# Optimization experiments

Measured on AMD Instinct MI355X. Metric: run time of the kernel, lower is better.

## Reference

```python
import jax, jax.numpy as jnp
import numpy as np

B, N, M, NSAMPLE = 16, 16384, 1024, 32
RADIUS = 0.1


def setup_inputs() -> dict:
    key = jax.random.key(0)
    xyz = jax.random.uniform(key, (B, N, 3), dtype=jnp.float32)
    return {"xyz": xyz}


def _furthest_point_sample(xyz, m):
    # xyz: [B, N, 3] -> indices [B, m], sequential max-min-distance selection.
    b, n, _ = xyz.shape

    def step(carry, _):
        mindist, far = carry  # [B, N], [B]
        cent = jnp.take_along_axis(xyz, far[:, None, None], axis=1)  # [B,1,3]
        d = jnp.sum((xyz - cent) ** 2, axis=-1)  # [B, N]
        mindist = jnp.minimum(mindist, d)
        nxt = jnp.argmax(mindist, axis=-1).astype(jnp.int32)
        return (mindist, nxt), far

    init = (jnp.full((b, n), 1e10, dtype=xyz.dtype), jnp.zeros((b,), jnp.int32))
    _, idx = jax.lax.scan(step, init, None, length=m)  # [m, B]
    return idx.T  # [B, m]


def _ball_query(xyz, centroids, radius, nsample):
    # PointNet++ semantics: first `nsample` points (in index order) within
    # radius of each centroid; short lists padded with the first hit.
    n = xyz.shape[1]
    dist2 = jnp.sum((centroids[:, :, None, :] - xyz[:, None, :, :]) ** 2, axis=-1)  # [B,M,N]
    key = jnp.where(dist2 < radius * radius, jnp.arange(n, dtype=jnp.int32), n)
    # nsample smallest keys in ascending index order
    neg_top, _ = jax.lax.top_k(-key, nsample)
    idx = -neg_top  # [B, M, nsample], ascending
    valid = idx < n
    idx = jnp.where(valid, idx, idx[..., :1])  # pad with first hit
    return idx


def reference(xyz):
    fps_idx = _furthest_point_sample(xyz, M)  # [B, M]
    centroids = jnp.take_along_axis(xyz, fps_idx[..., None], axis=1)  # [B, M, 3]
    idx = _ball_query(xyz, centroids, RADIUS, NSAMPLE)  # [B, M, nsample]
    grouped = jax.vmap(lambda p, i: p[i])(xyz, idx)  # [B, M, nsample, 3]
    grouped = grouped - centroids[:, :, None, :]  # use_xyz=True relative coords
    return grouped, centroids
```

## Files before the change

kernel.cpp:

```cpp
#include <hip/hip_runtime.h>

#define BATCH 16
#define NPTS 16384
#define MCENT 1024
#define NSAMPLE 32

__global__ __launch_bounds__(1024) void fps_kernel(const float* __restrict__ xyz,
                                                   float* __restrict__ cent_out) {
#pragma clang fp contract(off)
    const int b = blockIdx.x;
    const int tid = threadIdx.x;
    const int lane = tid & 63;
    const int wid = tid >> 6;
    const float* xb = xyz + (size_t)b * NPTS * 3;
    float* cb = cent_out + (size_t)b * MCENT * 3;

    float px[16], py[16], pz[16], md[16];
#pragma unroll
    for (int j = 0; j < 16; ++j) {
        int p = j * 1024 + tid;
        px[j] = xb[p * 3 + 0];
        py[j] = xb[p * 3 + 1];
        pz[j] = xb[p * 3 + 2];
        md[j] = 1e10f;
    }

    __shared__ float redv[16];
    __shared__ int   redi[16];
    __shared__ int   cur_sh;

    int cur = 0;
    for (int m = 0; m < MCENT; ++m) {
        int c = __builtin_amdgcn_readfirstlane(cur);
        float cx = xb[c * 3 + 0];
        float cy = xb[c * 3 + 1];
        float cz = xb[c * 3 + 2];
        if (tid == 0) {
            cb[m * 3 + 0] = cx;
            cb[m * 3 + 1] = cy;
            cb[m * 3 + 2] = cz;
        }
        float bv = -1.0f;
        int bi = 0x7fffffff;
#pragma unroll
        for (int j = 0; j < 16; ++j) {
            float dx = px[j] - cx;
            float dy = py[j] - cy;
            float dz = pz[j] - cz;
            float d = dx * dx + dy * dy;
            d = d + dz * dz;
            float nm = fminf(md[j], d);
            md[j] = nm;
            if (nm > bv) { bv = nm; bi = j * 1024 + tid; }
        }
#pragma unroll
        for (int off = 32; off >= 1; off >>= 1) {
            float ov = __shfl_xor(bv, off);
            int   oi = __shfl_xor(bi, off);
            if (ov > bv || (ov == bv && oi < bi)) { bv = ov; bi = oi; }
        }
        if (lane == 0) { redv[wid] = bv; redi[wid] = bi; }
        __syncthreads();
        if (wid == 0) {
            float v = (lane < 16) ? redv[lane] : -1.0f;
            int   i = (lane < 16) ? redi[lane] : 0x7fffffff;
#pragma unroll
            for (int off = 8; off >= 1; off >>= 1) {
                float ov = __shfl_xor(v, off);
                int   oi = __shfl_xor(i, off);
                if (ov > v || (ov == v && oi < i)) { v = ov; i = oi; }
            }
            if (lane == 0) cur_sh = i;
        }
        __syncthreads();
        cur = cur_sh;
    }
}

__global__ __launch_bounds__(256) void ballq_kernel(const float* __restrict__ xyz,
                                                    const float* __restrict__ cent,
                                                    float* __restrict__ grouped) {
#pragma clang fp contract(off)
    const int lane = threadIdx.x & 63;
    const int wib = threadIdx.x >> 6;
    const int cid = blockIdx.x * 4 + wib;
    const int b = cid >> 10;
    const float* xb = xyz + (size_t)b * NPTS * 3;
    const float* c = cent + (size_t)cid * 3;
    float cx = c[0], cy = c[1], cz = c[2];
    float* g = grouped + (size_t)cid * NSAMPLE * 3;

    const float R2 = (float)(0.1 * 0.1);

    int total = 0;
    int first_p = -1;

    for (int p0 = 0; p0 < NPTS && total < NSAMPLE; p0 += 64) {
        int p = p0 + lane;
        float x = xb[p * 3 + 0];
        float y = xb[p * 3 + 1];
        float z = xb[p * 3 + 2];
        float dx = x - cx;
        float dy = y - cy;
        float dz = z - cz;
        float d = dx * dx + dy * dy;
        d = d + dz * dz;
        bool hit = d < R2;
        unsigned long long mask = __ballot(hit);
        if (hit) {
            unsigned int mb = __builtin_amdgcn_mbcnt_lo((unsigned int)mask, 0u);
            mb = __builtin_amdgcn_mbcnt_hi((unsigned int)(mask >> 32), mb);
            int pos = total + (int)mb;
            if (pos < NSAMPLE) {
                g[pos * 3 + 0] = dx;
                g[pos * 3 + 1] = dy;
                g[pos * 3 + 2] = dz;
            }
        }
        if (first_p < 0 && mask != 0ull) first_p = p0 + __builtin_ctzll(mask);
        total += __popcll(mask);
    }

    int sel = total < NSAMPLE ? total : NSAMPLE;
    if (sel < NSAMPLE) {
        float fx = xb[first_p * 3 + 0] - cx;
        float fy = xb[first_p * 3 + 1] - cy;
        float fz = xb[first_p * 3 + 2] - cz;
        int s = lane;
        if (s >= sel && s < NSAMPLE) {
            g[s * 3 + 0] = fx;
            g[s * 3 + 1] = fy;
            g[s * 3 + 2] = fz;
        }
    }
}

extern "C" void kernel_launch(void* const* d_in, const int* in_sizes, int n_in,
                              void* d_out, int out_size, void* d_ws, size_t ws_size,
                              hipStream_t stream) {
    const float* xyz = (const float*)d_in[0];
    float* out = (float*)d_out;
    float* grouped = out;
    float* cent = out + (size_t)BATCH * MCENT * NSAMPLE * 3;

    fps_kernel<<<BATCH, 1024, 0, stream>>>(xyz, cent);
    ballq_kernel<<<(BATCH * MCENT) / 4, 256, 0, stream>>>(xyz, cent, grouped);
}
```

Measured before the change: 2.626 ms.

## Morton-sort points and skip FPS updates for distant thread bounding boxes

Adds a per-batch Morton bucket sort that writes points (with original indices) into workspace so each thread owns a spatially compact group of 16 points. In FPS, each thread keeps a bounding box and skips the distance update when the box's lower-bound distance to the new centroid cannot lower its current max-min distance, and wavefronts with no active threads reuse their cached reduction result. The winning centroid's coordinates travel through the reduction, which drops a global load, and the reduction buffers are double-buffered so one barrier per iteration suffices. The cost is an extra kernel launch, extra shuffles per reduction step, and reliance on the 0.999 slack and index tie-breaks to keep selection identical to the reference.

```diff
diff --git a/kernel.cpp b/kernel.cpp
--- a/kernel.cpp
+++ b/kernel.cpp
@@ -4,76 +4,189 @@
 #define NPTS 16384
 #define MCENT 1024
 #define NSAMPLE 32
+#define PPT 16
+
+__device__ __forceinline__ unsigned morton10(float x, float y, float z) {
+    int qx = (int)(x * 16.0f); qx = qx < 0 ? 0 : (qx > 15 ? 15 : qx);
+    int qy = (int)(y * 8.0f);  qy = qy < 0 ? 0 : (qy > 7 ? 7 : qy);
+    int qz = (int)(z * 8.0f);  qz = qz < 0 ? 0 : (qz > 7 ? 7 : qz);
+    unsigned c = 0;
+    c |= (unsigned)(qx & 1) | ((unsigned)(qy & 1) << 1) | ((unsigned)(qz & 1) << 2);
+    c |= (((unsigned)(qx >> 1) & 1) << 3) | (((unsigned)(qy >> 1) & 1) << 4) | (((unsigned)(qz >> 1) & 1) << 5);
+    c |= (((unsigned)(qx >> 2) & 1) << 6) | (((unsigned)(qy >> 2) & 1) << 7) | (((unsigned)(qz >> 2) & 1) << 8);
+    c |= (((unsigned)(qx >> 3) & 1) << 9);
+    return c;
+}
+
+__global__ __launch_bounds__(1024) void sort_kernel(const float* __restrict__ xyz,
+                                                    float4* __restrict__ sorted) {
+    const int b = blockIdx.x;
+    const int tid = threadIdx.x;
+    const int lane = tid & 63;
+    const int wid = tid >> 6;
+    const float* xb = xyz + (size_t)b * NPTS * 3;
+    float4* sb = sorted + (size_t)b * NPTS;
+
+    __shared__ unsigned hist[1024];
+    __shared__ unsigned wsum[16];
+    hist[tid] = 0;
+    __syncthreads();
+
+    float mx[16], my[16], mz[16];
+    unsigned mc[16];
+#pragma unroll
+    for (int j = 0; j < 16; ++j) {
+        int p = j * 1024 + tid;
+        mx[j] = xb[p * 3 + 0];
+        my[j] = xb[p * 3 + 1];
+        mz[j] = xb[p * 3 + 2];
+        mc[j] = morton10(mx[j], my[j], mz[j]);
+        atomicAdd(&hist[mc[j]], 1u);
+    }
+    __syncthreads();
+
+    unsigned orig = hist[tid];
+    unsigned v = orig;
+#pragma unroll
+    for (int off = 1; off < 64; off <<= 1) {
+        unsigned n = __shfl_up(v, off);
+        if (lane >= off) v += n;
+    }
+    if (lane == 63) wsum[wid] = v;
+    __syncthreads();
+    if (wid == 0 && lane < 16) {
+        unsigned s = wsum[lane];
+#pragma unroll
+        for (int off = 1; off < 16; off <<= 1) {
+            unsigned n = __shfl_up(s, off);
+            if (lane >= off) s += n;
+        }
+        wsum[lane] = s;
+    }
+    __syncthreads();
+    unsigned base = v - orig + (wid > 0 ? wsum[wid - 1] : 0u);
+    __syncthreads();
+    hist[tid] = base;
+    __syncthreads();
+
+#pragma unroll
+    for (int j = 0; j < 16; ++j) {
+        int p = j * 1024 + tid;
+        unsigned pos = atomicAdd(&hist[mc[j]], 1u);
+        sb[pos] = make_float4(mx[j], my[j], mz[j], __int_as_float(p));
+    }
+}
 
 __global__ __launch_bounds__(1024) void fps_kernel(const float* __restrict__ xyz,
+                                                   const float4* __restrict__ sorted,
                                                    float* __restrict__ cent_out) {
 #pragma clang fp contract(off)
     const int b = blockIdx.x;
     const int tid = threadIdx.x;
     const int lane = tid & 63;
     const int wid = tid >> 6;
+    const float4* sb = sorted + (size_t)b * NPTS;
     const float* xb = xyz + (size_t)b * NPTS * 3;
     float* cb = cent_out + (size_t)b * MCENT * 3;
 
-    float px[16], py[16], pz[16], md[16];
-#pragma unroll
-    for (int j = 0; j < 16; ++j) {
-        int p = j * 1024 + tid;
-        px[j] = xb[p * 3 + 0];
-        py[j] = xb[p * 3 + 1];
-        pz[j] = xb[p * 3 + 2];
+    float px[PPT], py[PPT], pz[PPT], md[PPT];
+    int pid[PPT];
+    float blx = 1e30f, bly = 1e30f, blz = 1e30f;
+    float bhx = -1e30f, bhy = -1e30f, bhz = -1e30f;
+#pragma unroll
+    for (int j = 0; j < PPT; ++j) {
+        float4 v = sb[tid * PPT + j];
+        px[j] = v.x; py[j] = v.y; pz[j] = v.z;
+        pid[j] = __float_as_int(v.w);
         md[j] = 1e10f;
-    }
-
-    __shared__ float redv[16];
-    __shared__ int   redi[16];
-    __shared__ int   cur_sh;
-
-    int cur = 0;
+        blx = fminf(blx, v.x); bhx = fmaxf(bhx, v.x);
+        bly = fminf(bly, v.y); bhy = fmaxf(bhy, v.y);
+        blz = fminf(blz, v.z); bhz = fmaxf(bhz, v.z);
+    }
+
+    __shared__ float redv[2][16], redx[2][16], redy[2][16], redz[2][16];
+    __shared__ int redi[2][16];
+
+    float cx = xb[0], cy = xb[1], cz = xb[2];
+
+    float bv = -1.0f; int bi = 0x7fffffff;
+    float bxc = 0.f, byc = 0.f, bzc = 0.f;
+    float wv = -1.0f; int wi = 0x7fffffff;
+    float wx = 0.f, wy = 0.f, wz = 0.f;
+
     for (int m = 0; m < MCENT; ++m) {
-        int c = __builtin_amdgcn_readfirstlane(cur);
-        float cx = xb[c * 3 + 0];
-        float cy = xb[c * 3 + 1];
-        float cz = xb[c * 3 + 2];
         if (tid == 0) {
             cb[m * 3 + 0] = cx;
             cb[m * 3 + 1] = cy;
             cb[m * 3 + 2] = cz;
         }
-        float bv = -1.0f;
-        int bi = 0x7fffffff;
-#pragma unroll
-        for (int j = 0; j < 16; ++j) {
-            float dx = px[j] - cx;
-            float dy = py[j] - cy;
-            float dz = pz[j] - cz;
-            float d = dx * dx + dy * dy;
-            d = d + dz * dz;
-            float nm = fminf(md[j], d);
-            md[j] = nm;
-            if (nm > bv) { bv = nm; bi = j * 1024 + tid; }
-        }
-#pragma unroll
-        for (int off = 32; off >= 1; off >>= 1) {
-            float ov = __shfl_xor(bv, off);
-            int   oi = __shfl_xor(bi, off);
-            if (ov > bv || (ov == bv && oi < bi)) { bv = ov; bi = oi; }
-        }
-        if (lane == 0) { redv[wid] = bv; redi[wid] = bi; }
-        __syncthreads();
-        if (wid == 0) {
-            float v = (lane < 16) ? redv[lane] : -1.0f;
-            int   i = (lane < 16) ? redi[lane] : 0x7fffffff;
-#pragma unroll
-            for (int off = 8; off >= 1; off >>= 1) {
+        if (m == MCENT - 1) break;
+
+        float tx = fmaxf(fmaxf(blx - cx, cx - bhx), 0.0f);
+        float ty = fmaxf(fmaxf(bly - cy, cy - bhy), 0.0f);
+        float tz = fmaxf(fmaxf(blz - cz, cz - bhz), 0.0f);
+        float lb = tx * tx + ty * ty + tz * tz;
+        bool active = (m == 0) || (lb * 0.999f < bv);
+
+        if (active) {
+            bv = -1.0f; bi = 0x7fffffff;
+#pragma unroll
+            for (int j = 0; j < PPT; ++j) {
+                float dx = px[j] - cx;
+                float dy = py[j] - cy;
+                float dz = pz[j] - cz;
+                float d = dx * dx + dy * dy;
+                d = d + dz * dz;
+                float nm = fminf(md[j], d);
+                md[j] = nm;
+                if (nm > bv || (nm == bv && pid[j] < bi)) {
+                    bv = nm; bi = pid[j];
+                    bxc = px[j]; byc = py[j]; bzc = pz[j];
+                }
+            }
+        }
+
+        unsigned long long act = __ballot(active);
+        if (act != 0ull) {
+            float v = bv; int i = bi;
+            float x = bxc, y = byc, z = bzc;
+#pragma unroll
+            for (int off = 32; off >= 1; off >>= 1) {
                 float ov = __shfl_xor(v, off);
                 int   oi = __shfl_xor(i, off);
-                if (ov > v || (ov == v && oi < i)) { v = ov; i = oi; }
+                float ox = __shfl_xor(x, off);
+                float oy = __shfl_xor(y, off);
+                float oz = __shfl_xor(z, off);
+                if (ov > v || (ov == v && oi < i)) { v = ov; i = oi; x = ox; y = oy; z = oz; }
             }
-            if (lane == 0) cur_sh = i;
+            wv = v; wi = i; wx = x; wy = y; wz = z;
+        }
+        const int pb = m & 1;
+        if (lane == 0) {
+            redv[pb][wid] = wv; redi[pb][wid] = wi;
+            redx[pb][wid] = wx; redy[pb][wid] = wy; redz[pb][wid] = wz;
         }
         __syncthreads();
-        cur = cur_sh;
+
+        float v; int i; float x, y, z;
+        if (lane < 16) {
+            v = redv[pb][lane]; i = redi[pb][lane];
+            x = redx[pb][lane]; y = redy[pb][lane]; z = redz[pb][lane];
+        } else {
+            v = -1.0f; i = 0x7fffffff; x = 0.f; y = 0.f; z = 0.f;
+        }
+#pragma unroll
+        for (int off = 8; off >= 1; off >>= 1) {
+            float ov = __shfl_xor(v, off);
+            int   oi = __shfl_xor(i, off);
+            float ox = __shfl_xor(x, off);
+            float oy = __shfl_xor(y, off);
+            float oz = __shfl_xor(z, off);
+            if (ov > v || (ov == v && oi < i)) { v = ov; i = oi; x = ox; y = oy; z = oz; }
+        }
+        cx = __shfl(x, 0);
+        cy = __shfl(y, 0);
+        cz = __shfl(z, 0);
     }
 }
 
@@ -142,7 +255,9 @@
     float* out = (float*)d_out;
     float* grouped = out;
     float* cent = out + (size_t)BATCH * MCENT * NSAMPLE * 3;
-
-    fps_kernel<<<BATCH, 1024, 0, stream>>>(xyz, cent);
+    float4* sorted = (float4*)d_ws;
+
+    sort_kernel<<<BATCH, 1024, 0, stream>>>(xyz, sorted);
+    fps_kernel<<<BATCH, 1024, 0, stream>>>(xyz, sorted, cent);
     ballq_kernel<<<(BATCH * MCENT) / 4, 256, 0, stream>>>(xyz, cent, grouped);
 }
```

After: 3.787 ms. 44.2% more time.
